# Kernel optimization log

Hardware: AMD Instinct MI355X
Metric: run time of the kernel (lower is better)

The kernel has to match this reference:

```python
import jax, jax.numpy as jnp
import numpy as np
import math

N, C3, T = 32, 192, 2048  # C3 = 3 * head_dim

def setup_inputs() -> dict:
    key = jax.random.key(0)
    qkv = jax.random.normal(key, (N, C3, T), dtype=jnp.float32)
    return {"qkv": qkv}

def reference(qkv):
    ch = qkv.shape[1] // 3
    q, k, v = jnp.split(qkv, 3, axis=1)              # each [N, C, T]
    scale = 1.0 / math.sqrt(math.sqrt(ch))           # applied to both q and k
    # [N, T, T] attention scores
    weight = jnp.einsum('bct,bcs->bts', q * scale, k * scale)
    weight = jax.nn.softmax(weight.astype(jnp.float32), axis=-1).astype(qkv.dtype)
    # [N, C, T] output
    return jnp.einsum('bts,bcs->bct', weight, v)
```

## Files before the change

kernel.cpp:

```cpp
#include <hip/hip_runtime.h>

#define T_DIM 2048
#define D_DIM 64
#define NB 32

#define QT_OFF 0
#define KB_OFF 4194304
#define VB_OFF 8388608

typedef _Float16 half8 __attribute__((ext_vector_type(8)));
typedef _Float16 half4 __attribute__((ext_vector_type(4)));
typedef float f32x16 __attribute__((ext_vector_type(16)));
typedef float f32x4 __attribute__((ext_vector_type(4)));

#define ZERO16 (f32x16){0.f,0.f,0.f,0.f,0.f,0.f,0.f,0.f,0.f,0.f,0.f,0.f,0.f,0.f,0.f,0.f}

__global__ __launch_bounds__(256) void prepass(const float* __restrict__ qkv,
                                               _Float16* __restrict__ ws) {
  const int ttile = blockIdx.x;
  const int b = blockIdx.y;
  const int type = blockIdx.z;
  const int t0 = ttile * 64;
  __shared__ float Ls[64][65];

  const int tid = threadIdx.x;
  const int cc = tid >> 4;
  const int tt = (tid & 15) << 2;
  const float QS = 0.125f * 1.4426950408889634f;
  const float* src = qkv + ((size_t)b * 192 + type * 64) * T_DIM;
#pragma unroll
  for (int p = 0; p < 4; ++p) {
    const int c = p * 16 + cc;
    float4 v = *(const float4*)&src[(size_t)c * T_DIM + t0 + tt];
    if (type == 0) { v.x *= QS; v.y *= QS; v.z *= QS; v.w *= QS; }
    Ls[c][tt] = v.x; Ls[c][tt + 1] = v.y; Ls[c][tt + 2] = v.z; Ls[c][tt + 3] = v.w;
  }
  __syncthreads();

  if (type == 0) {
    const int t = tid >> 2, cg = (tid & 3) * 16;
    half8 h0, h1;
#pragma unroll
    for (int j = 0; j < 8; ++j) h0[j] = (_Float16)Ls[cg + j][t];
#pragma unroll
    for (int j = 0; j < 8; ++j) h1[j] = (_Float16)Ls[cg + 8 + j][t];
    _Float16* dst = ws + QT_OFF + ((size_t)b * T_DIM + t0 + t) * 64 + cg;
    *(half8*)dst = h0;
    *(half8*)(dst + 8) = h1;
  } else if (type == 1) {
    const int f = tid >> 6, h = (tid >> 5) & 1, s31 = tid & 31;
#pragma unroll
    for (int sbl = 0; sbl < 2; ++sbl) {
      const int sb = (t0 >> 5) + sbl;
      half8 hv;
#pragma unroll
      for (int j = 0; j < 8; ++j) hv[j] = (_Float16)Ls[f * 16 + h * 8 + j][sbl * 32 + s31];
      _Float16* dst = ws + KB_OFF + ((size_t)b * 64 + sb) * 2048 + f * 512 + h * 256 + s31 * 8;
      *(half8*)dst = hv;
    }
  } else {
#pragma unroll
    for (int p = 0; p < 2; ++p) {
      const int g = p * 256 + tid;
      const int sgl = g >> 6, c = g & 63;
      half8 hv;
#pragma unroll
      for (int j = 0; j < 8; ++j) hv[j] = (_Float16)Ls[c][sgl * 8 + j];
      _Float16* dst = ws + VB_OFF + (((size_t)b * 256 + (t0 >> 3) + sgl) * 64 + c) * 8;
      *(half8*)dst = hv;
    }
  }
}

static __device__ __forceinline__ half4 shflx32(half4 x) {
  int2 i = __builtin_bit_cast(int2, x);
  i.x = __shfl_xor(i.x, 32);
  i.y = __shfl_xor(i.y, 32);
  return __builtin_bit_cast(half4, i);
}
static __device__ __forceinline__ half8 cat4(half4 lo, half4 hi) {
  half8 r;
  r[0] = lo[0]; r[1] = lo[1]; r[2] = lo[2]; r[3] = lo[3];
  r[4] = hi[0]; r[5] = hi[1]; r[6] = hi[2]; r[7] = hi[3];
  return r;
}

__global__ __launch_bounds__(256, 2) void qkv_main(const _Float16* __restrict__ ws,
                                                   float* __restrict__ out) {
  const int tid = threadIdx.x;
  const int wave = tid >> 6, lane = tid & 63;
  const int l31 = lane & 31, h = lane >> 5;
  const int b = blockIdx.x & 31;
  const int qg = blockIdx.x >> 5;
  const int t0 = qg * 128 + wave * 32;

  const _Float16* Qt = ws + QT_OFF;
  const _Float16* kbase = ws + KB_OFF + (size_t)b * 131072;
  const _Float16* vbase = ws + VB_OFF + (size_t)b * 131072;

  const _Float16* qp = Qt + ((size_t)b * T_DIM + t0 + l31) * 64 + h * 8;
  half8 bq[4];
#pragma unroll
  for (int f = 0; f < 4; ++f) bq[f] = *(const half8*)(qp + f * 16);

  const f32x16 fz = ZERO16;
  f32x16 o0 = ZERO16, o1 = ZERO16;
  float lp = 0.f;

  const _Float16* kp = kbase + h * 256 + l31 * 8;
  const _Float16* vp = vbase + h * 512 + l31 * 8;

  half8 ak[4], bv[4];
#pragma unroll
  for (int f = 0; f < 4; ++f) ak[f] = *(const half8*)(kp + f * 512);
  bv[0] = *(const half8*)(vp);
  bv[1] = *(const half8*)(vp + 256);
  bv[2] = *(const half8*)(vp + 1024);
  bv[3] = *(const half8*)(vp + 1280);

  for (int sb = 0; sb < 64; ++sb) {
    const size_t nxt = (size_t)(sb + 1 < 64 ? sb + 1 : sb) * 2048;
    const _Float16* kn = kp + nxt;
    half8 an0 = *(const half8*)(kn);
    half8 an1 = *(const half8*)(kn + 512);
    half8 an2 = *(const half8*)(kn + 1024);
    half8 an3 = *(const half8*)(kn + 1536);
    const _Float16* vn = vp + nxt;
    half8 bn0 = *(const half8*)(vn);
    half8 bn1 = *(const half8*)(vn + 256);
    half8 bn2 = *(const half8*)(vn + 1024);
    half8 bn3 = *(const half8*)(vn + 1280);

    f32x16 s;
    s = __builtin_amdgcn_mfma_f32_32x32x16_f16(ak[0], bq[0], fz, 0, 0, 0);
    s = __builtin_amdgcn_mfma_f32_32x32x16_f16(ak[1], bq[1], s, 0, 0, 0);
    s = __builtin_amdgcn_mfma_f32_32x32x16_f16(ak[2], bq[2], s, 0, 0, 0);
    s = __builtin_amdgcn_mfma_f32_32x32x16_f16(ak[3], bq[3], s, 0, 0, 0);

    half4 ap[4];
#pragma unroll
    for (int g = 0; g < 4; ++g) {
      const float e0 = __builtin_amdgcn_exp2f(s[4 * g + 0]);
      const float e1 = __builtin_amdgcn_exp2f(s[4 * g + 1]);
      const float e2 = __builtin_amdgcn_exp2f(s[4 * g + 2]);
      const float e3 = __builtin_amdgcn_exp2f(s[4 * g + 3]);
      lp += (e0 + e1) + (e2 + e3);
      ap[g] = (half4){(_Float16)e0, (_Float16)e1, (_Float16)e2, (_Float16)e3};
    }

    const half4 xs0 = h ? ap[0] : ap[1];
    const half4 ot0 = shflx32(xs0);
    const half8 A0 = cat4(h ? ot0 : ap[0], h ? ap[1] : ot0);
    const half4 xs1 = h ? ap[2] : ap[3];
    const half4 ot1 = shflx32(xs1);
    const half8 A1 = cat4(h ? ot1 : ap[2], h ? ap[3] : ot1);

    o0 = __builtin_amdgcn_mfma_f32_32x32x16_f16(A0, bv[0], o0, 0, 0, 0);
    o1 = __builtin_amdgcn_mfma_f32_32x32x16_f16(A0, bv[1], o1, 0, 0, 0);
    o0 = __builtin_amdgcn_mfma_f32_32x32x16_f16(A1, bv[2], o0, 0, 0, 0);
    o1 = __builtin_amdgcn_mfma_f32_32x32x16_f16(A1, bv[3], o1, 0, 0, 0);

    ak[0] = an0; ak[1] = an1; ak[2] = an2; ak[3] = an3;
    bv[0] = bn0; bv[1] = bn1; bv[2] = bn2; bv[3] = bn3;
  }

  const float lf = lp + __shfl_xor(lp, 32);
  const float linv = 1.0f / lf;
  float* ob = out + (size_t)b * D_DIM * T_DIM;
#pragma unroll
  for (int g = 0; g < 4; ++g) {
    f32x4 r0, r1;
#pragma unroll
    for (int j = 0; j < 4; ++j) {
      const float il = __shfl(linv, g * 8 + h * 4 + j);
      r0[j] = o0[g * 4 + j] * il;
      r1[j] = o1[g * 4 + j] * il;
    }
    const int q = t0 + g * 8 + h * 4;
    *(f32x4*)&ob[(size_t)l31 * T_DIM + q] = r0;
    *(f32x4*)&ob[(size_t)(32 + l31) * T_DIM + q] = r1;
  }
}

extern "C" void kernel_launch(void* const* d_in, const int* in_sizes, int n_in,
                              void* d_out, int out_size, void* d_ws, size_t ws_size,
                              hipStream_t stream) {
  const float* qkv = (const float*)d_in[0];
  float* out = (float*)d_out;
  _Float16* ws = (_Float16*)d_ws;
  hipLaunchKernelGGL(prepass, dim3(32, 32, 3), dim3(256), 0, stream, qkv, ws);
  hipLaunchKernelGGL(qkv_main, dim3(512), dim3(256), 0, stream, ws, out);
}
```

Before: 137.9 us.

## Stage K/V tiles through double-buffered shared memory shared by all waves

```diff
diff --git a/kernel.cpp b/kernel.cpp
--- a/kernel.cpp
+++ b/kernel.cpp
@@ -94,6 +94,8 @@
   const int qg = blockIdx.x >> 5;
   const int t0 = qg * 128 + wave * 32;
 
+  __shared__ _Float16 kv[2][4096];
+
   const _Float16* Qt = ws + QT_OFF;
   const _Float16* kbase = ws + KB_OFF + (size_t)b * 131072;
   const _Float16* vbase = ws + VB_OFF + (size_t)b * 131072;
@@ -107,35 +109,40 @@
   f32x16 o0 = ZERO16, o1 = ZERO16;
   float lp = 0.f;
 
-  const _Float16* kp = kbase + h * 256 + l31 * 8;
-  const _Float16* vp = vbase + h * 512 + l31 * 8;
-
-  half8 ak[4], bv[4];
-#pragma unroll
-  for (int f = 0; f < 4; ++f) ak[f] = *(const half8*)(kp + f * 512);
-  bv[0] = *(const half8*)(vp);
-  bv[1] = *(const half8*)(vp + 256);
-  bv[2] = *(const half8*)(vp + 1024);
-  bv[3] = *(const half8*)(vp + 1280);
+  {
+    half8 gk = *(const half8*)(kbase + tid * 8);
+    half8 gv = *(const half8*)(vbase + tid * 8);
+    *(half8*)&kv[0][tid * 8] = gk;
+    *(half8*)&kv[0][2048 + tid * 8] = gv;
+  }
+
+  const int koff = lane * 8;
+  const int voff = h * 512 + l31 * 8;
 
   for (int sb = 0; sb < 64; ++sb) {
-    const size_t nxt = (size_t)(sb + 1 < 64 ? sb + 1 : sb) * 2048;
-    const _Float16* kn = kp + nxt;
-    half8 an0 = *(const half8*)(kn);
-    half8 an1 = *(const half8*)(kn + 512);
-    half8 an2 = *(const half8*)(kn + 1024);
-    half8 an3 = *(const half8*)(kn + 1536);
-    const _Float16* vn = vp + nxt;
-    half8 bn0 = *(const half8*)(vn);
-    half8 bn1 = *(const half8*)(vn + 256);
-    half8 bn2 = *(const half8*)(vn + 1024);
-    half8 bn3 = *(const half8*)(vn + 1280);
+    const int cur = sb & 1;
+    __syncthreads();
+
+    const int sn = (sb + 1 < 64) ? sb + 1 : 63;
+    half8 gk = *(const half8*)(kbase + (size_t)sn * 2048 + tid * 8);
+    half8 gv = *(const half8*)(vbase + (size_t)sn * 2048 + tid * 8);
+
+    const _Float16* sK = &kv[cur][0];
+    const _Float16* sV = &kv[cur][2048];
+    half8 ak0 = *(const half8*)&sK[koff];
+    half8 ak1 = *(const half8*)&sK[koff + 512];
+    half8 ak2 = *(const half8*)&sK[koff + 1024];
+    half8 ak3 = *(const half8*)&sK[koff + 1536];
+    half8 bv0 = *(const half8*)&sV[voff];
+    half8 bv1 = *(const half8*)&sV[voff + 256];
+    half8 bv2 = *(const half8*)&sV[voff + 1024];
+    half8 bv3 = *(const half8*)&sV[voff + 1280];
 
     f32x16 s;
-    s = __builtin_amdgcn_mfma_f32_32x32x16_f16(ak[0], bq[0], fz, 0, 0, 0);
-    s = __builtin_amdgcn_mfma_f32_32x32x16_f16(ak[1], bq[1], s, 0, 0, 0);
-    s = __builtin_amdgcn_mfma_f32_32x32x16_f16(ak[2], bq[2], s, 0, 0, 0);
-    s = __builtin_amdgcn_mfma_f32_32x32x16_f16(ak[3], bq[3], s, 0, 0, 0);
+    s = __builtin_amdgcn_mfma_f32_32x32x16_f16(ak0, bq[0], fz, 0, 0, 0);
+    s = __builtin_amdgcn_mfma_f32_32x32x16_f16(ak1, bq[1], s, 0, 0, 0);
+    s = __builtin_amdgcn_mfma_f32_32x32x16_f16(ak2, bq[2], s, 0, 0, 0);
+    s = __builtin_amdgcn_mfma_f32_32x32x16_f16(ak3, bq[3], s, 0, 0, 0);
 
     half4 ap[4];
 #pragma unroll
@@ -155,13 +162,13 @@
     const half4 ot1 = shflx32(xs1);
     const half8 A1 = cat4(h ? ot1 : ap[2], h ? ap[3] : ot1);
 
-    o0 = __builtin_amdgcn_mfma_f32_32x32x16_f16(A0, bv[0], o0, 0, 0, 0);
-    o1 = __builtin_amdgcn_mfma_f32_32x32x16_f16(A0, bv[1], o1, 0, 0, 0);
-    o0 = __builtin_amdgcn_mfma_f32_32x32x16_f16(A1, bv[2], o0, 0, 0, 0);
-    o1 = __builtin_amdgcn_mfma_f32_32x32x16_f16(A1, bv[3], o1, 0, 0, 0);
-
-    ak[0] = an0; ak[1] = an1; ak[2] = an2; ak[3] = an3;
-    bv[0] = bn0; bv[1] = bn1; bv[2] = bn2; bv[3] = bn3;
+    o0 = __builtin_amdgcn_mfma_f32_32x32x16_f16(A0, bv0, o0, 0, 0, 0);
+    o1 = __builtin_amdgcn_mfma_f32_32x32x16_f16(A0, bv1, o1, 0, 0, 0);
+    o0 = __builtin_amdgcn_mfma_f32_32x32x16_f16(A1, bv2, o0, 0, 0, 0);
+    o1 = __builtin_amdgcn_mfma_f32_32x32x16_f16(A1, bv3, o1, 0, 0, 0);
+
+    *(half8*)&kv[cur ^ 1][tid * 8] = gk;
+    *(half8*)&kv[cur ^ 1][2048 + tid * 8] = gv;
   }
 
   const float lf = lp + __shfl_xor(lp, 32);
```

Measured after the change: 137.0 us. About the same (-0.6%).

## Permute K layout in prepass to remove cross-lane shuffles of P

Applied to the files above, without the earlier changes.

```diff
diff --git a/kernel.cpp b/kernel.cpp
--- a/kernel.cpp
+++ b/kernel.cpp
@@ -49,13 +49,15 @@
     *(half8*)(dst + 8) = h1;
   } else if (type == 1) {
     const int f = tid >> 6, h = (tid >> 5) & 1, s31 = tid & 31;
+    const int u = (s31 >> 2) & 3;
+    const int m31 = s31 ^ ((((u ^ (u >> 1)) & 1) != 0) ? 12 : 0);
 #pragma unroll
     for (int sbl = 0; sbl < 2; ++sbl) {
       const int sb = (t0 >> 5) + sbl;
       half8 hv;
 #pragma unroll
       for (int j = 0; j < 8; ++j) hv[j] = (_Float16)Ls[f * 16 + h * 8 + j][sbl * 32 + s31];
-      _Float16* dst = ws + KB_OFF + ((size_t)b * 64 + sb) * 2048 + f * 512 + h * 256 + s31 * 8;
+      _Float16* dst = ws + KB_OFF + ((size_t)b * 64 + sb) * 2048 + f * 512 + h * 256 + m31 * 8;
       *(half8*)dst = hv;
     }
   } else {
@@ -70,19 +72,6 @@
       *(half8*)dst = hv;
     }
   }
-}
-
-static __device__ __forceinline__ half4 shflx32(half4 x) {
-  int2 i = __builtin_bit_cast(int2, x);
-  i.x = __shfl_xor(i.x, 32);
-  i.y = __shfl_xor(i.y, 32);
-  return __builtin_bit_cast(half4, i);
-}
-static __device__ __forceinline__ half8 cat4(half4 lo, half4 hi) {
-  half8 r;
-  r[0] = lo[0]; r[1] = lo[1]; r[2] = lo[2]; r[3] = lo[3];
-  r[4] = hi[0]; r[5] = hi[1]; r[6] = hi[2]; r[7] = hi[3];
-  return r;
 }
 
 __global__ __launch_bounds__(256, 2) void qkv_main(const _Float16* __restrict__ ws,
@@ -118,6 +107,7 @@
   bv[2] = *(const half8*)(vp + 1024);
   bv[3] = *(const half8*)(vp + 1280);
 
+#pragma unroll 2
   for (int sb = 0; sb < 64; ++sb) {
     const size_t nxt = (size_t)(sb + 1 < 64 ? sb + 1 : sb) * 2048;
     const _Float16* kn = kp + nxt;
@@ -137,23 +127,17 @@
     s = __builtin_amdgcn_mfma_f32_32x32x16_f16(ak[2], bq[2], s, 0, 0, 0);
     s = __builtin_amdgcn_mfma_f32_32x32x16_f16(ak[3], bq[3], s, 0, 0, 0);
 
-    half4 ap[4];
+    float es[16];
 #pragma unroll
-    for (int g = 0; g < 4; ++g) {
-      const float e0 = __builtin_amdgcn_exp2f(s[4 * g + 0]);
-      const float e1 = __builtin_amdgcn_exp2f(s[4 * g + 1]);
-      const float e2 = __builtin_amdgcn_exp2f(s[4 * g + 2]);
-      const float e3 = __builtin_amdgcn_exp2f(s[4 * g + 3]);
-      lp += (e0 + e1) + (e2 + e3);
-      ap[g] = (half4){(_Float16)e0, (_Float16)e1, (_Float16)e2, (_Float16)e3};
-    }
+    for (int g = 0; g < 16; ++g) es[g] = __builtin_amdgcn_exp2f(s[g]);
+    lp += (((es[0] + es[1]) + (es[2] + es[3])) + ((es[4] + es[5]) + (es[6] + es[7]))) +
+          (((es[8] + es[9]) + (es[10] + es[11])) + ((es[12] + es[13]) + (es[14] + es[15])));
 
-    const half4 xs0 = h ? ap[0] : ap[1];
-    const half4 ot0 = shflx32(xs0);
-    const half8 A0 = cat4(h ? ot0 : ap[0], h ? ap[1] : ot0);
-    const half4 xs1 = h ? ap[2] : ap[3];
-    const half4 ot1 = shflx32(xs1);
-    const half8 A1 = cat4(h ? ot1 : ap[2], h ? ap[3] : ot1);
+    half8 A0, A1;
+#pragma unroll
+    for (int j = 0; j < 8; ++j) A0[j] = (_Float16)es[j];
+#pragma unroll
+    for (int j = 0; j < 8; ++j) A1[j] = (_Float16)es[8 + j];
 
     o0 = __builtin_amdgcn_mfma_f32_32x32x16_f16(A0, bv[0], o0, 0, 0, 0);
     o1 = __builtin_amdgcn_mfma_f32_32x32x16_f16(A0, bv[1], o1, 0, 0, 0);
```

Measured after the change: 132.4 us. 4.0% less time.
